# Kernel optimization log

Hardware: AMD Instinct MI355X
Metric: run time of the kernel (lower is better)

The kernel has to match this reference:

```python
import jax, jax.numpy as jnp
import numpy as np

DIM = 1024
HEADS = 16
HEAD_DIM = DIM // HEADS
HIDDEN = DIM * 4
EPS = 1e-6


def _layernorm(x, g, b):
    mu = jnp.mean(x, axis=-1, keepdims=True)
    var = jnp.mean(jnp.square(x - mu), axis=-1, keepdims=True)
    return (x - mu) * jax.lax.rsqrt(var + EPS) * g + b


def setup_inputs() -> dict:
    key = jax.random.key(0)
    ks = jax.random.split(key, 12)
    s = 0.02
    return {
        "x": jax.random.normal(ks[0], (16, 1024, DIM), dtype=jnp.float32),
        "ln1_g": jnp.ones((DIM,), jnp.float32),
        "ln1_b": jnp.zeros((DIM,), jnp.float32),
        "qkv_w": jax.random.normal(ks[1], (DIM, 3 * DIM), jnp.float32) * s,
        "qkv_b": jnp.zeros((3 * DIM,), jnp.float32),
        "proj_w": jax.random.normal(ks[2], (DIM, DIM), jnp.float32) * s,
        "proj_b": jnp.zeros((DIM,), jnp.float32),
        "ls1_g": jnp.ones((DIM,), jnp.float32),
        "ln2_g": jnp.ones((DIM,), jnp.float32),
        "ln2_b": jnp.zeros((DIM,), jnp.float32),
        "fc1_w": jax.random.normal(ks[3], (DIM, HIDDEN), jnp.float32) * s,
        "fc1_b": jnp.zeros((HIDDEN,), jnp.float32),
        "fc2_w": jax.random.normal(ks[4], (HIDDEN, DIM), jnp.float32) * s,
        "fc2_b": jnp.zeros((DIM,), jnp.float32),
        "ls2_g": jnp.ones((DIM,), jnp.float32),
    }


def reference(x, ln1_g, ln1_b, qkv_w, qkv_b, proj_w, proj_b, ls1_g,
              ln2_g, ln2_b, fc1_w, fc1_b, fc2_w, fc2_b, ls2_g):
    B, N, C = x.shape
    # --- attention branch (NOTE: original code omits 1/sqrt(d) scaling) ---
    h = _layernorm(x, ln1_g, ln1_b)
    qkv = (h @ qkv_w + qkv_b).reshape(B, N, 3, HEADS, HEAD_DIM)
    q, k, v = jnp.moveaxis(qkv, 2, 0)          # each [B, N, H, D]
    attn = jnp.einsum("bqhd,bkhd->bhqk", q, k)  # no scale, faithful to source
    attn = jax.nn.softmax(attn, axis=-1)
    out = jnp.einsum("bhqk,bkhd->bqhd", attn, v).reshape(B, N, C)
    x = x + (out @ proj_w + proj_b) * ls1_g
    # --- MLP branch ---
    h = _layernorm(x, ln2_g, ln2_b)
    h = jax.nn.gelu(h @ fc1_w + fc1_b, approximate=False)
    x = x + (h @ fc2_w + fc2_b) * ls2_g
    return x
```

## Files before the change

kernel.cpp:

```cpp
#include <hip/hip_runtime.h>
#include <hip/hip_bf16.h>
#include <math.h>

typedef __attribute__((ext_vector_type(8))) short short8;
typedef __attribute__((ext_vector_type(4))) float f32x4;

#define MFMA16(a,b,c) __builtin_amdgcn_mfma_f32_16x16x32_bf16((a),(b),(c),0,0,0)

__device__ __forceinline__ unsigned short f2bf(float f){
  unsigned int u = __builtin_bit_cast(unsigned int, f);
  u += 0x7fffu + ((u >> 16) & 1u);
  return (unsigned short)(u >> 16);
}
__device__ __forceinline__ unsigned short f2bf_rn(float f){
  unsigned int u = __builtin_bit_cast(unsigned int, f);
  return (unsigned short)((u + 0x8000u) >> 16);
}
__device__ __forceinline__ float bf2f(unsigned short u){
  unsigned int v = ((unsigned int)u) << 16;
  return __builtin_bit_cast(float, v);
}
__device__ __forceinline__ float exp2fast(float x){
  return __builtin_amdgcn_exp2f(x);
}

__device__ __forceinline__ void gload16(const void* g, void* lds){
  __builtin_amdgcn_global_load_lds(
      (const __attribute__((address_space(1))) unsigned int*)g,
      (__attribute__((address_space(3))) unsigned int*)lds, 16, 0, 0);
}

__global__ __launch_bounds__(256) void k_transpose_cast(const float* __restrict__ in,
    unsigned short* __restrict__ out, int K, int N)
{
  __shared__ unsigned short tile[32][33];
  const int tx = threadIdx.x, ty = threadIdx.y;
  const int n0 = blockIdx.x * 32, k0 = blockIdx.y * 32;
  #pragma unroll
  for (int i = 0; i < 4; i++) {
    int k = k0 + ty + i*8;
    tile[ty + i*8][tx] = f2bf(in[(size_t)k * N + n0 + tx]);
  }
  __syncthreads();
  #pragma unroll
  for (int i = 0; i < 4; i++) {
    int n = n0 + ty + i*8;
    out[(size_t)n * K + k0 + tx] = tile[tx][ty + i*8];
  }
}

template<int BF16IN>
__global__ __launch_bounds__(256) void k_layernorm(const void* __restrict__ xin,
    const float* __restrict__ g, const float* __restrict__ b,
    unsigned short* __restrict__ out)
{
  const int row = blockIdx.x;
  const int t = threadIdx.x;
  float4 v;
  if (BF16IN) {
    const ushort4 u = ((const ushort4*)((const unsigned short*)xin + (size_t)row * 1024))[t];
    v.x = bf2f(u.x); v.y = bf2f(u.y); v.z = bf2f(u.z); v.w = bf2f(u.w);
  } else {
    v = ((const float4*)((const float*)xin + (size_t)row * 1024))[t];
  }
  float s  = v.x + v.y + v.z + v.w;
  float s2 = v.x*v.x + v.y*v.y + v.z*v.z + v.w*v.w;
  #pragma unroll
  for (int m = 1; m < 64; m <<= 1) {
    s  += __shfl_xor(s,  m);
    s2 += __shfl_xor(s2, m);
  }
  __shared__ float red[2][4];
  const int wid = t >> 6, lane = t & 63;
  if (lane == 0) { red[0][wid] = s; red[1][wid] = s2; }
  __syncthreads();
  s  = red[0][0] + red[0][1] + red[0][2] + red[0][3];
  s2 = red[1][0] + red[1][1] + red[1][2] + red[1][3];
  const float mu = s * (1.0f / 1024.0f);
  const float var = s2 * (1.0f / 1024.0f) - mu * mu;
  const float rstd = rsqrtf(var + 1e-6f);
  const float4 gv = ((const float4*)g)[t];
  const float4 bv = ((const float4*)b)[t];
  ushort4 o;
  o.x = f2bf((v.x - mu) * rstd * gv.x + bv.x);
  o.y = f2bf((v.y - mu) * rstd * gv.y + bv.y);
  o.z = f2bf((v.z - mu) * rstd * gv.z + bv.z);
  o.w = f2bf((v.w - mu) * rstd * gv.w + bv.w);
  ((ushort4*)(out + (size_t)row * 1024))[t] = o;
}

template<int EPI>
__global__ __launch_bounds__(256, 4) void k_gemm128(
    const unsigned short* __restrict__ A,
    const unsigned short* __restrict__ Bt,
    const float* __restrict__ bias,
    const void* __restrict__ resid,
    const float* __restrict__ lsg,
    void* __restrict__ outp,
    unsigned short* __restrict__ vtp,
    int M, int N, int K, int nbn)
{
  __shared__ __align__(16) unsigned short Asm[128 * 64];
  __shared__ __align__(16) unsigned short Bsm[128 * 64];

  const int bid = blockIdx.x;
  const int mrows = (gridDim.x >> 3) / nbn;
  const int xcd = bid & 7, l = bid >> 3;
  const int bm = xcd * mrows + (l % mrows);
  const int bn = l / mrows;

  const int t = threadIdx.x, lane = t & 63;
  const int wid = t >> 6, wm = wid >> 1, wn = wid & 1;
  const int fr = lane & 15, fg = lane >> 4;

  size_t aOf[4], bOf[4];
  int dOf[4];
  #pragma unroll
  for (int i = 0; i < 4; i++) {
    const int s = i * 256 + t;
    const int row = s >> 3, c = s & 7;
    const int cs = c ^ (row & 7);
    dOf[i] = s * 16;
    aOf[i] = ((size_t)bm * 128 + row) * K + cs * 8;
    bOf[i] = ((size_t)bn * 128 + row) * K + cs * 8;
  }

  f32x4 acc[4][4] = {};

  for (int kt = 0; kt < K; kt += 64) {
    __syncthreads();
    #pragma unroll
    for (int i = 0; i < 4; i++) gload16(A  + aOf[i] + kt, (char*)Asm + dOf[i]);
    #pragma unroll
    for (int i = 0; i < 4; i++) gload16(Bt + bOf[i] + kt, (char*)Bsm + dOf[i]);
    __syncthreads();

    #pragma unroll
    for (int kk = 0; kk < 2; kk++) {
      short8 af[4], bfv[4];
      #pragma unroll
      for (int m = 0; m < 4; m++) {
        const int row = wm * 64 + m * 16 + fr;
        af[m] = *(const short8*)((const char*)Asm + row * 128
                                 + (((kk*4 + fg) ^ (row & 7)) * 16));
      }
      #pragma unroll
      for (int n = 0; n < 4; n++) {
        const int row = wn * 64 + n * 16 + fr;
        bfv[n] = *(const short8*)((const char*)Bsm + row * 128
                                  + (((kk*4 + fg) ^ (row & 7)) * 16));
      }
      __builtin_amdgcn_s_setprio(1);
      #pragma unroll
      for (int m = 0; m < 4; m++)
        #pragma unroll
        for (int n = 0; n < 4; n++)
          acc[m][n] = MFMA16(af[m], bfv[n], acc[m][n]);
      __builtin_amdgcn_s_setprio(0);
    }
  }

  const int row0 = bm * 128 + wm * 64 + fg * 4;
  const int col0 = bn * 128 + wn * 64 + fr;
  #pragma unroll
  for (int n = 0; n < 4; n++) {
    const int col = col0 + n * 16;
    const float bcol = bias[col];
    float lscale = 0.f;
    if (EPI >= 2) lscale = lsg[col];
    #pragma unroll
    for (int m = 0; m < 4; m++) {
      #pragma unroll
      for (int r = 0; r < 4; r++) {
        const int row = row0 + m * 16 + r;
        float v = acc[m][n][r] + bcol;
        if (EPI == 0) {
          if (bn < 16) {
            if (col < 1024) v *= 1.44269504088896340736f;
            ((unsigned short*)outp)[(size_t)row * 2048 + col] = f2bf(v);
          } else {
            const int d = col - 2048, hh = d >> 6, dd = d & 63;
            const int bb = row >> 10, nn = row & 1023;
            vtp[(((size_t)bb * 16 + hh) * 64 + dd) * 1024 + nn] = f2bf(v);
          }
        } else if (EPI == 1) {
          const float u = v * (0.7978845608f + 0.0356774081f * v * v);
          v = v * __builtin_amdgcn_rcpf(1.0f + __expf(-2.0f * u));
          ((unsigned short*)outp)[(size_t)row * N + col] = f2bf(v);
        } else if (EPI == 2) {
          const float rv = ((const float*)resid)[(size_t)row * N + col];
          ((unsigned short*)outp)[(size_t)row * N + col] = f2bf(rv + v * lscale);
        } else {
          const float rv = bf2f(((const unsigned short*)resid)[(size_t)row * N + col]);
          ((float*)outp)[(size_t)row * N + col] = rv + v * lscale;
        }
      }
    }
  }
}

__global__ __launch_bounds__(512) void k_attn(const unsigned short* __restrict__ qk,
                                              const unsigned short* __restrict__ vT,
                                              unsigned short* __restrict__ out)
{
  const int bid = blockIdx.x;
  const int xcd = bid & 7, l = bid >> 3;
  const int bh = xcd * 32 + (l >> 2);
  const int qt = l & 3;
  const int b = bh >> 4, h = bh & 15;
  const int t = threadIdx.x, lane = t & 63, wid = t >> 6;
  const int fr = lane & 15, fg = lane >> 4;
  const int q0 = qt * 256 + wid * 32;

  __shared__ __align__(16) unsigned short Ksm[2][64 * 64];
  __shared__ __align__(16) unsigned short Vsm[2][64 * 64];
  __shared__ __align__(16) unsigned short plds[8][16][72];

  const size_t qbase = (size_t)b * 1024 * 2048 + (size_t)h * 64;
  const size_t kbase = qbase + 1024;
  const size_t vbase = (size_t)bh * 64 * 1024;

  short8 qf[2][2];
  #pragma unroll
  for (int m = 0; m < 2; m++)
    #pragma unroll
    for (int kh = 0; kh < 2; kh++)
      qf[m][kh] = *(const short8*)(qk + qbase + (size_t)(q0 + m*16 + fr) * 2048
                                   + kh*32 + fg*8);

  short8 ones;
  #pragma unroll
  for (int i = 0; i < 8; i++) ones[i] = (short)0x3F80;

  f32x4 oacc[2][4] = {};
  f32x4 lacc[2] = {};
  float mrow[2][4];
  #pragma unroll
  for (int m = 0; m < 2; m++)
    #pragma unroll
    for (int r = 0; r < 4; r++) mrow[m][r] = -1e30f;

  const int srow = t >> 3, sc = t & 7;
  const int scs = sc ^ (srow & 7);
  const unsigned short* kSrc = qk + kbase + (size_t)srow * 2048 + scs*8;
  const unsigned short* vSrc = vT + vbase + (size_t)srow * 1024 + scs*8;

  gload16(kSrc, (char*)&Ksm[0][0] + t*16);
  gload16(vSrc, (char*)&Vsm[0][0] + t*16);
  __syncthreads();

  for (int it = 0; it < 16; ++it) {
    const int buf = it & 1;
    if (it < 15) {
      gload16(kSrc + (size_t)(it + 1) * 64 * 2048, (char*)&Ksm[buf ^ 1][0] + t*16);
      gload16(vSrc + (it + 1) * 64,                (char*)&Vsm[buf ^ 1][0] + t*16);
    }

    f32x4 sacc[2][4] = {};
    #pragma unroll
    for (int n = 0; n < 4; n++) {
      #pragma unroll
      for (int kh = 0; kh < 2; kh++) {
        const int krow = n*16 + fr;
        short8 kf = *(const short8*)&Ksm[buf][krow*64 + (((kh*4 + fg) ^ (krow & 7)) * 8)];
        sacc[0][n] = MFMA16(qf[0][kh], kf, sacc[0][n]);
        sacc[1][n] = MFMA16(qf[1][kh], kf, sacc[1][n]);
      }
    }

    short8 pf[2][2];
    #pragma unroll
    for (int m = 0; m < 2; m++) {
      float pm[4];
      #pragma unroll
      for (int r = 0; r < 4; r++)
        pm[r] = fmaxf(fmaxf(sacc[m][0][r], sacc[m][1][r]),
                      fmaxf(sacc[m][2][r], sacc[m][3][r]));
      #pragma unroll
      for (int msk = 1; msk < 16; msk <<= 1)
        #pragma unroll
        for (int r = 0; r < 4; r++) pm[r] = fmaxf(pm[r], __shfl_xor(pm[r], msk));

      int grow = 0;
      #pragma unroll
      for (int r = 0; r < 4; r++) grow |= (pm[r] > mrow[m][r] + 11.5f) ? 1 : 0;
      if (__any(grow)) {
        #pragma unroll
        for (int r = 0; r < 4; r++) {
          const float mn = fmaxf(mrow[m][r], pm[r]);
          const float corr = exp2fast(mrow[m][r] - mn);
          mrow[m][r] = mn;
          lacc[m][r] *= corr;
          #pragma unroll
          for (int d16 = 0; d16 < 4; d16++) oacc[m][d16][r] *= corr;
        }
      }

      #pragma unroll
      for (int n = 0; n < 4; n++)
        #pragma unroll
        for (int r = 0; r < 4; r++)
          plds[wid][fg*4 + r][n*16 + fr] =
              f2bf_rn(exp2fast(sacc[m][n][r] - mrow[m][r]));
      #pragma unroll
      for (int kh = 0; kh < 2; kh++)
        pf[m][kh] = *(const short8*)&plds[wid][fr][kh*32 + fg*8];
    }

    #pragma unroll
    for (int m = 0; m < 2; m++)
      #pragma unroll
      for (int kh = 0; kh < 2; kh++)
        lacc[m] = MFMA16(pf[m][kh], ones, lacc[m]);

    #pragma unroll
    for (int d16 = 0; d16 < 4; d16++) {
      #pragma unroll
      for (int kh = 0; kh < 2; kh++) {
        const int vrow = d16*16 + fr;
        short8 vf = *(const short8*)&Vsm[buf][vrow*64 + (((kh*4 + fg) ^ (vrow & 7)) * 8)];
        oacc[0][d16] = MFMA16(pf[0][kh], vf, oacc[0][d16]);
        oacc[1][d16] = MFMA16(pf[1][kh], vf, oacc[1][d16]);
      }
    }

    __syncthreads();
  }

  #pragma unroll
  for (int m = 0; m < 2; m++) {
    float inv[4];
    #pragma unroll
    for (int r = 0; r < 4; r++) inv[r] = __builtin_amdgcn_rcpf(lacc[m][r]);
    #pragma unroll
    for (int d16 = 0; d16 < 4; d16++) {
      #pragma unroll
      for (int r = 0; r < 4; r++) {
        const int qrow = q0 + m*16 + fg*4 + r;
        const int col = h*64 + d16*16 + fr;
        out[(size_t)(b * 1024 + qrow) * 1024 + col] = f2bf(oacc[m][d16][r] * inv[r]);
      }
    }
  }
}

extern "C" void kernel_launch(void* const* d_in, const int* in_sizes, int n_in,
                              void* d_out, int out_size, void* d_ws, size_t ws_size,
                              hipStream_t stream) {
  const float* x      = (const float*)d_in[0];
  const float* ln1_g  = (const float*)d_in[1];
  const float* ln1_b  = (const float*)d_in[2];
  const float* qkv_w  = (const float*)d_in[3];
  const float* qkv_b  = (const float*)d_in[4];
  const float* proj_w = (const float*)d_in[5];
  const float* proj_b = (const float*)d_in[6];
  const float* ls1_g  = (const float*)d_in[7];
  const float* ln2_g  = (const float*)d_in[8];
  const float* ln2_b  = (const float*)d_in[9];
  const float* fc1_w  = (const float*)d_in[10];
  const float* fc1_b  = (const float*)d_in[11];
  const float* fc2_w  = (const float*)d_in[12];
  const float* fc2_b  = (const float*)d_in[13];
  const float* ls2_g  = (const float*)d_in[14];

  char* w = (char*)d_ws;
  unsigned short* wqkvT  = (unsigned short*)(w + 0);
  unsigned short* wprojT = (unsigned short*)(w + 6291456);
  unsigned short* wfc1T  = (unsigned short*)(w + 8388608);
  unsigned short* wfc2T  = (unsigned short*)(w + 16777216);
  unsigned short* x1     = (unsigned short*)(w + 25165824);
  unsigned short* h1     = (unsigned short*)(w + 58720256);
  unsigned short* qkbuf  = (unsigned short*)(w + 92274688);
  unsigned short* vtbuf  = (unsigned short*)(w + 159383552);
  unsigned short* attno  = (unsigned short*)(w + 192937984);
  unsigned short* h3     = (unsigned short*)(w + 92274688);

  dim3 tb32(32, 8);
  k_transpose_cast<<<dim3(3072/32, 1024/32), tb32, 0, stream>>>(qkv_w,  wqkvT, 1024, 3072);
  k_transpose_cast<<<dim3(1024/32, 1024/32), tb32, 0, stream>>>(proj_w, wprojT, 1024, 1024);
  k_transpose_cast<<<dim3(4096/32, 1024/32), tb32, 0, stream>>>(fc1_w,  wfc1T, 1024, 4096);
  k_transpose_cast<<<dim3(1024/32, 4096/32), tb32, 0, stream>>>(fc2_w,  wfc2T, 4096, 1024);

  k_layernorm<0><<<16384, 256, 0, stream>>>(x, ln1_g, ln1_b, h1);
  k_gemm128<0><<<128*24, 256, 0, stream>>>(h1, wqkvT, qkv_b, nullptr, nullptr,
                                           qkbuf, vtbuf, 16384, 3072, 1024, 24);
  k_attn<<<1024, 512, 0, stream>>>(qkbuf, vtbuf, attno);
  k_gemm128<2><<<128*8, 256, 0, stream>>>(attno, wprojT, proj_b, x, ls1_g,
                                          x1, nullptr, 16384, 1024, 1024, 8);
  k_layernorm<1><<<16384, 256, 0, stream>>>(x1, ln2_g, ln2_b, h1);
  k_gemm128<1><<<128*32, 256, 0, stream>>>(h1, wfc1T, fc1_b, nullptr, nullptr,
                                           h3, nullptr, 16384, 4096, 1024, 32);
  k_gemm128<3><<<128*8, 256, 0, stream>>>(h3, wfc2T, fc2_b, x1, ls2_g,
                                          (float*)d_out, nullptr, 16384, 1024, 4096, 8);
}
```

Measured before the change: 733.8 us.

## Double-buffer GEMM K tiles in LDS with BK=32 to overlap loads and MFMA

The 128x128 GEMM main loop now uses two 32-wide K stages in shared memory instead of one 64-wide stage. The next tile's global-to-LDS loads are issued before the MFMAs on the current tile, with one barrier per iteration instead of two. This aims to hide global load latency behind compute, at the cost of twice as many loop iterations, less work per barrier, and a new XOR swizzle for the narrower rows that may cause LDS bank conflicts.

New measurement: 797.6 us. +8.7%, slower.

```diff
diff --git a/kernel.cpp b/kernel.cpp
--- a/kernel.cpp
+++ b/kernel.cpp
@@ -100,8 +100,8 @@
     unsigned short* __restrict__ vtp,
     int M, int N, int K, int nbn)
 {
-  __shared__ __align__(16) unsigned short Asm[128 * 64];
-  __shared__ __align__(16) unsigned short Bsm[128 * 64];
+  __shared__ __align__(16) unsigned short Asm[2][128 * 32];
+  __shared__ __align__(16) unsigned short Bsm[2][128 * 32];
 
   const int bid = blockIdx.x;
   const int mrows = (gridDim.x >> 3) / nbn;
@@ -113,51 +113,56 @@
   const int wid = t >> 6, wm = wid >> 1, wn = wid & 1;
   const int fr = lane & 15, fg = lane >> 4;
 
-  size_t aOf[4], bOf[4];
-  int dOf[4];
-  #pragma unroll
-  for (int i = 0; i < 4; i++) {
-    const int s = i * 256 + t;
-    const int row = s >> 3, c = s & 7;
-    const int cs = c ^ (row & 7);
-    dOf[i] = s * 16;
-    aOf[i] = ((size_t)bm * 128 + row) * K + cs * 8;
-    bOf[i] = ((size_t)bn * 128 + row) * K + cs * 8;
-  }
+  const int s0 = t, s1 = 256 + t;
+  const int r0 = s0 >> 2, cs0 = ((s0 & 3) ^ ((r0 >> 1) & 3));
+  const int r1 = s1 >> 2, cs1 = ((s1 & 3) ^ ((r1 >> 1) & 3));
+  const int d0 = s0 * 16, d1 = s1 * 16;
+  const size_t a0 = ((size_t)bm * 128 + r0) * K + cs0 * 8;
+  const size_t a1 = ((size_t)bm * 128 + r1) * K + cs1 * 8;
+  const size_t b0 = ((size_t)bn * 128 + r0) * K + cs0 * 8;
+  const size_t b1 = ((size_t)bn * 128 + r1) * K + cs1 * 8;
 
   f32x4 acc[4][4] = {};
 
-  for (int kt = 0; kt < K; kt += 64) {
+  gload16(A  + a0, (char*)&Asm[0][0] + d0);
+  gload16(A  + a1, (char*)&Asm[0][0] + d1);
+  gload16(Bt + b0, (char*)&Bsm[0][0] + d0);
+  gload16(Bt + b1, (char*)&Bsm[0][0] + d1);
+  __syncthreads();
+
+  const int NT = K >> 5;
+  for (int it = 0; it < NT; ++it) {
+    const int buf = it & 1;
+    const size_t kofs = (size_t)(it + 1) * 32;
+    if (it + 1 < NT) {
+      gload16(A  + a0 + kofs, (char*)&Asm[buf ^ 1][0] + d0);
+      gload16(A  + a1 + kofs, (char*)&Asm[buf ^ 1][0] + d1);
+      gload16(Bt + b0 + kofs, (char*)&Bsm[buf ^ 1][0] + d0);
+      gload16(Bt + b1 + kofs, (char*)&Bsm[buf ^ 1][0] + d1);
+    }
+
+    short8 af[4], bfv[4];
+    #pragma unroll
+    for (int m = 0; m < 4; m++) {
+      const int row = wm * 64 + m * 16 + fr;
+      af[m] = *(const short8*)((const char*)&Asm[buf][0] + row * 64
+                               + ((fg ^ ((row >> 1) & 3)) * 16));
+    }
+    #pragma unroll
+    for (int n = 0; n < 4; n++) {
+      const int row = wn * 64 + n * 16 + fr;
+      bfv[n] = *(const short8*)((const char*)&Bsm[buf][0] + row * 64
+                                + ((fg ^ ((row >> 1) & 3)) * 16));
+    }
+    __builtin_amdgcn_s_setprio(1);
+    #pragma unroll
+    for (int m = 0; m < 4; m++)
+      #pragma unroll
+      for (int n = 0; n < 4; n++)
+        acc[m][n] = MFMA16(af[m], bfv[n], acc[m][n]);
+    __builtin_amdgcn_s_setprio(0);
+
     __syncthreads();
-    #pragma unroll
-    for (int i = 0; i < 4; i++) gload16(A  + aOf[i] + kt, (char*)Asm + dOf[i]);
-    #pragma unroll
-    for (int i = 0; i < 4; i++) gload16(Bt + bOf[i] + kt, (char*)Bsm + dOf[i]);
-    __syncthreads();
-
-    #pragma unroll
-    for (int kk = 0; kk < 2; kk++) {
-      short8 af[4], bfv[4];
-      #pragma unroll
-      for (int m = 0; m < 4; m++) {
-        const int row = wm * 64 + m * 16 + fr;
-        af[m] = *(const short8*)((const char*)Asm + row * 128
-                                 + (((kk*4 + fg) ^ (row & 7)) * 16));
-      }
-      #pragma unroll
-      for (int n = 0; n < 4; n++) {
-        const int row = wn * 64 + n * 16 + fr;
-        bfv[n] = *(const short8*)((const char*)Bsm + row * 128
-                                  + (((kk*4 + fg) ^ (row & 7)) * 16));
-      }
-      __builtin_amdgcn_s_setprio(1);
-      #pragma unroll
-      for (int m = 0; m < 4; m++)
-        #pragma unroll
-        for (int n = 0; n < 4; n++)
-          acc[m][n] = MFMA16(af[m], bfv[n], acc[m][n]);
-      __builtin_amdgcn_s_setprio(0);
-    }
   }
 
   const int row0 = bm * 128 + wm * 64 + fg * 4;
```
